# Performance work log

Hardware: AMD Instinct MI355X
Metric: run time of the kernel (lower is better)

Reference implementation:

```python
import jax, jax.numpy as jnp
import numpy as np

B, NOBJ, QD, VD = 128, 36, 2400, 2048
N = B * NOBJ
NEG_SLOPE = 0.2


def _edges():
    # fully connected per image, self-loops included (PyG GATConv adds them)
    base = np.arange(NOBJ)
    src = np.repeat(base, NOBJ)
    dst = np.tile(base, NOBJ)
    off = (np.arange(B) * NOBJ)[:, None]
    return np.stack([(src[None] + off).reshape(-1), (dst[None] + off).reshape(-1)])


def setup_inputs() -> dict:
    key = jax.random.key(0)
    ks = jax.random.split(key, 24)
    p = lambda k, shape, fan: jax.random.normal(k, shape, jnp.float32) * (1.0 / np.sqrt(fan))
    inp = {
        "question_embedding": jax.random.normal(ks[0], (B, QD), jnp.float32),
        "object_features": jax.random.normal(ks[1], (N, VD), jnp.float32),
        "edge_index": jnp.asarray(_edges(), jnp.int32),
        "Wq": p(ks[2], (QD, 2048), QD), "bq": jnp.zeros((2048,), jnp.float32),
        "Wv": p(ks[3], (VD, 2048), VD), "bv": jnp.zeros((2048,), jnp.float32),
        "W1": p(ks[4], (2048, 4 * 256), 2048), "a1s": p(ks[5], (4, 256), 256),
        "a1d": p(ks[6], (4, 256), 256), "b1": jnp.zeros((1024,), jnp.float32),
        "W2": p(ks[7], (1024, 4 * 256), 1024), "a2s": p(ks[8], (4, 256), 256),
        "a2d": p(ks[9], (4, 256), 256), "b2": jnp.zeros((1024,), jnp.float32),
        "W3": p(ks[10], (1024, 5 * 512), 1024), "a3s": p(ks[11], (5, 512), 512),
        "a3d": p(ks[12], (5, 512), 512), "b3": jnp.zeros((512,), jnp.float32),
        "batch_size": B, "num_obj": NOBJ,
    }
    return inp


def gat_conv(x, edge_index, W, a_src, a_dst, b, heads, ch, concat):
    n = x.shape[0]
    h = (x @ W).reshape(n, heads, ch)                       # [N,H,C]
    src, dst = edge_index[0], edge_index[1]
    al_s = jnp.einsum('nhc,hc->nh', h, a_src)               # [N,H]
    al_d = jnp.einsum('nhc,hc->nh', h, a_dst)
    e = jax.nn.leaky_relu(al_s[src] + al_d[dst], NEG_SLOPE)  # [E,H]
    # segment softmax over edges sharing a destination node
    e_max = jax.ops.segment_max(e, dst, num_segments=n)
    e = jnp.exp(e - e_max[dst])
    denom = jax.ops.segment_sum(e, dst, num_segments=n)
    alpha = e / (denom[dst] + 1e-16)                        # [E,H]
    msg = h[src] * alpha[:, :, None]                        # [E,H,C]
    out = jax.ops.segment_sum(msg, dst, num_segments=n)     # [N,H,C]
    out = out.reshape(n, heads * ch) if concat else out.mean(axis=1)
    return out + b


def reference(question_embedding, object_features, edge_index,
              Wq, bq, Wv, bv,
              W1, a1s, a1d, b1,
              W2, a2s, a2d, b2,
              W3, a3s, a3d, b3,
              batch_size, num_obj):
    # hadamard fusion of question with per-object features
    q = question_embedding @ Wq + bq                        # [B,2048]
    q = jnp.repeat(q, num_obj, axis=0)                      # [N,2048]
    v = object_features @ Wv + bv
    x = q * v
    g1 = jax.nn.relu(gat_conv(x, edge_index, W1, a1s, a1d, b1, 4, 256, True))
    g2 = jax.nn.relu(gat_conv(g1, edge_index, W2, a2s, a2d, b2, 4, 256, True))
    g2 = g2 + g1                                            # residual
    return gat_conv(g2, edge_index, W3, a3s, a3d, b3, 5, 512, False)
```

## Files before the change

kernel.cpp:

```cpp
#include <hip/hip_runtime.h>
#include <hip/hip_bf16.h>

typedef unsigned short u16;
typedef __bf16 bf16x8 __attribute__((ext_vector_type(8)));
typedef float f32x4 __attribute__((ext_vector_type(4)));

#define B_IMG 128
#define NOBJ  36
#define NNODE (B_IMG * NOBJ)

__device__ __forceinline__ float b2f(u16 u) {
    union { unsigned int i; float f; } v; v.i = ((unsigned int)u) << 16; return v.f;
}
__device__ __forceinline__ u16 f2b(float f) {
    union { float f; unsigned int i; } v; v.f = f;
    unsigned int u = v.i;
    return (u16)((u + 0x7fffu + ((u >> 16) & 1u)) >> 16);
}

__global__ __launch_bounds__(256)
void conv_mat(const float* __restrict__ src, u16* __restrict__ dst, int n4) {
    const int i = blockIdx.x * 256 + threadIdx.x;
    if (i >= n4) return;
    const float4 f = ((const float4*)src)[i];
    ushort4 o; o.x = f2b(f.x); o.y = f2b(f.y); o.z = f2b(f.z); o.w = f2b(f.w);
    ((ushort4*)dst)[i] = o;
}

__global__ __launch_bounds__(256)
void transpose_cvt(const float* __restrict__ src, u16* __restrict__ dst, int R, int C) {
    __shared__ u16 tile[32][33];
    const int bx = blockIdx.x * 32, by = blockIdx.y * 32;
    const int tx = threadIdx.x & 31, ty = threadIdx.x >> 5;
    #pragma unroll
    for (int i = ty; i < 32; i += 8)
        tile[i][tx] = f2b(src[(size_t)(by + i) * C + bx + tx]);
    __syncthreads();
    #pragma unroll
    for (int i = ty; i < 32; i += 8) dst[(size_t)(bx + i) * R + by + tx] = tile[tx][i];
}

template<int EPI>
__global__ __launch_bounds__(256)
void gemm_tn(const u16* __restrict__ A, const u16* __restrict__ Bt,
             int M, int N, int K, int kLen,
             float* __restrict__ Cf, u16* __restrict__ Cb,
             const float* __restrict__ bias, const float* __restrict__ qmul)
{
    __shared__ __align__(16) u16 lds[3 * 8192];

    const int t    = threadIdx.x;
    const int lane = t & 63;
    const int wave = t >> 6;
    const int wr = wave >> 1, wc = wave & 1;
    const int quad = lane >> 4, l16 = lane & 15;
    const int rowBase = blockIdx.y * 128;
    const int colBase = blockIdx.x * 128;
    const int k0 = blockIdx.z * kLen;

    const u16* gA0 = A  + (size_t)(rowBase + wave * 32 + (lane >> 2)) * K + k0 + (lane & 3) * 8;
    const u16* gA1 = gA0 + 16 * (size_t)K;
    const u16* gB0 = Bt + (size_t)(colBase + wave * 32 + (lane >> 2)) * K + k0 + (lane & 3) * 8;
    const u16* gB1 = gB0 + 16 * (size_t)K;
    const int sO0 = (wave * 32 +  0) * 32;
    const int sO1 = (wave * 32 + 16) * 32;

    int afr[4], bfr[4];
    #pragma unroll
    for (int r = 0; r < 4; r++) afr[r] = (wr * 64 + r * 16 + l16) * 32 + quad * 8;
    #pragma unroll
    for (int c = 0; c < 4; c++) bfr[c] = 4096 + (wc * 64 + c * 16 + l16) * 32 + quad * 8;

    f32x4 acc[4][4];
    #pragma unroll
    for (int r = 0; r < 4; r++)
        #pragma unroll
        for (int c = 0; c < 4; c++)
            acc[r][c] = (f32x4){0.f, 0.f, 0.f, 0.f};

    auto dma_tile = [&](int it, int st) {
        const int kk = it * 32;
        const int bo = st * 8192;
        __builtin_amdgcn_global_load_lds(
            (const __attribute__((address_space(1))) void*)(gA0 + kk),
            (__attribute__((address_space(3))) void*)&lds[bo + sO0], 16, 0, 0);
        __builtin_amdgcn_global_load_lds(
            (const __attribute__((address_space(1))) void*)(gA1 + kk),
            (__attribute__((address_space(3))) void*)&lds[bo + sO1], 16, 0, 0);
        __builtin_amdgcn_global_load_lds(
            (const __attribute__((address_space(1))) void*)(gB0 + kk),
            (__attribute__((address_space(3))) void*)&lds[bo + 4096 + sO0], 16, 0, 0);
        __builtin_amdgcn_global_load_lds(
            (const __attribute__((address_space(1))) void*)(gB1 + kk),
            (__attribute__((address_space(3))) void*)&lds[bo + 4096 + sO1], 16, 0, 0);
    };

    const int nIter = kLen >> 5;
    dma_tile(0, 0);
    dma_tile(1, 1);

    int cur = 0;
    for (int it = 0; it < nIter; ++it) {
        if (it + 1 < nIter) {
            asm volatile("s_waitcnt vmcnt(4)\n\ts_barrier" ::: "memory");
        } else {
            asm volatile("s_waitcnt vmcnt(0)\n\ts_barrier" ::: "memory");
        }
        if (it + 2 < nIter) {
            const int st2 = (cur + 2 >= 3) ? cur - 1 : cur + 2;
            dma_tile(it + 2, st2);
        }
        const int bo = cur * 8192;
        bf16x8 avf[4], bvf[4];
        #pragma unroll
        for (int r = 0; r < 4; r++) avf[r] = *(const bf16x8*)&lds[afr[r] + bo];
        #pragma unroll
        for (int c = 0; c < 4; c++) bvf[c] = *(const bf16x8*)&lds[bfr[c] + bo];
        #pragma unroll
        for (int r = 0; r < 4; r++)
            #pragma unroll
            for (int c = 0; c < 4; c++)
                acc[r][c] = __builtin_amdgcn_mfma_f32_16x16x32_bf16(avf[r], bvf[c], acc[r][c], 0, 0, 0);
        cur = (cur + 1 == 3) ? 0 : cur + 1;
    }

    #pragma unroll
    for (int r = 0; r < 4; r++) {
        const int mBase = rowBase + wr * 64 + r * 16 + quad * 4;
        #pragma unroll
        for (int c = 0; c < 4; c++) {
            const int n = colBase + wc * 64 + c * 16 + l16;
            #pragma unroll
            for (int e = 0; e < 4; e++) {
                const int m = mBase + e;
                float v = acc[r][c][e];
                if (EPI == 1) {
                    Cf[((size_t)blockIdx.z * M + m) * N + n] = v;
                } else if (EPI == 2) {
                    v += bias[n];
                    v *= qmul[(size_t)(m / NOBJ) * N + n];
                    Cb[(size_t)m * N + n] = f2b(v);
                } else {
                    Cb[(size_t)m * N + n] = f2b(v);
                }
            }
        }
    }
}

__global__ __launch_bounds__(256)
void qcombine(const float* __restrict__ p, const float* __restrict__ bias,
              float* __restrict__ q, int MN, int S)
{
    const int i = blockIdx.x * 256 + threadIdx.x;
    float s = 0.f;
    for (int z = 0; z < S; z++) s += p[(size_t)z * MN + i];
    q[i] = s + bias[i & 2047];
}

template<int H, int C>
__global__ __launch_bounds__(H * 64)
void al_kernel(const u16* __restrict__ h, const float* __restrict__ a_s,
               const float* __restrict__ a_d, float* __restrict__ als, float* __restrict__ ald)
{
    const int n = blockIdx.x;
    const int wv = threadIdx.x >> 6, lane = threadIdx.x & 63;
    constexpr int PL = C / 64;
    const u16*   hp  = h   + (size_t)n * (H * C) + wv * C + lane * PL;
    const float* asp = a_s + wv * C + lane * PL;
    const float* adp = a_d + wv * C + lane * PL;
    u16 hb[PL];
    if constexpr (PL == 4) { *(uint2*)hb = *(const uint2*)hp; }
    else                   { *(uint4*)hb = *(const uint4*)hp; }
    float s1 = 0.f, s2 = 0.f;
    #pragma unroll
    for (int i = 0; i < PL; i++) {
        const float hv = b2f(hb[i]);
        s1 += hv * asp[i];
        s2 += hv * adp[i];
    }
    #pragma unroll
    for (int off = 32; off > 0; off >>= 1) {
        s1 += __shfl_down(s1, off);
        s2 += __shfl_down(s2, off);
    }
    if (lane == 0) { als[n * H + wv] = s1; ald[n * H + wv] = s2; }
}

template<int H, int C, int MODE>
__global__ __launch_bounds__(256)
void attn_kernel(const u16* __restrict__ h, const float* __restrict__ a_src,
                 const float* __restrict__ a_dst, const float* __restrict__ bias,
                 const u16* __restrict__ resid, u16* __restrict__ outb)
{
    __shared__ __align__(16) u16 hl[36 * C];
    __shared__ float alpha[36 * 36];
    __shared__ float asl[36], adl[36];
    __shared__ float psum[36][8][2];
    const int b = blockIdx.y, hd = blockIdx.x;
    const int t = threadIdx.x;
    const int nb = b * NOBJ;
    constexpr int CH = C / 8;
    for (int e = t; e < 36 * CH; e += 256) {
        const int row = e / CH, col = (e - row * CH) * 8;
        *(uint4*)&hl[row * C + col] = *(const uint4*)&h[(size_t)(nb + row) * (H * C) + hd * C + col];
    }
    __syncthreads();
    constexpr int SEG = C / 8;
    for (int e = t; e < 36 * 8; e += 256) {
        const int n = e >> 3, sg = e & 7;
        const u16*   hp = &hl[n * C + sg * SEG];
        const float* as = a_src + hd * C + sg * SEG;
        const float* ad = a_dst + hd * C + sg * SEG;
        float s1 = 0.f, s2 = 0.f;
        #pragma unroll 8
        for (int i = 0; i < SEG; i++) {
            const float hv = b2f(hp[i]);
            s1 += hv * as[i]; s2 += hv * ad[i];
        }
        psum[n][sg][0] = s1; psum[n][sg][1] = s2;
    }
    __syncthreads();
    if (t < 36) {
        float s1 = 0.f, s2 = 0.f;
        #pragma unroll
        for (int sg = 0; sg < 8; sg++) { s1 += psum[t][sg][0]; s2 += psum[t][sg][1]; }
        asl[t] = s1; adl[t] = s2;
    }
    __syncthreads();
    if (t < 36) {
        const float ad = adl[t];
        float mx = -1e30f;
        for (int s = 0; s < 36; s++) {
            float v = asl[s] + ad; v = (v > 0.f) ? v : 0.2f * v;
            alpha[t * 36 + s] = v; mx = fmaxf(mx, v);
        }
        float sum = 0.f;
        for (int s = 0; s < 36; s++) { const float ex = expf(alpha[t * 36 + s] - mx); alpha[t * 36 + s] = ex; sum += ex; }
        const float inv = 1.f / (sum + 1e-16f);
        for (int s = 0; s < 36; s++) alpha[t * 36 + s] *= inv;
    }
    __syncthreads();
    constexpr int NC4 = C / 4;
    for (int e = t; e < 36 * NC4; e += 256) {
        const int d = e / NC4, c4 = (e - d * NC4) * 4;
        float a0 = 0, a1 = 0, a2 = 0, a3 = 0;
        for (int s = 0; s < 36; s++) {
            const float al = alpha[d * 36 + s];
            const ushort4 hv = *(const ushort4*)&hl[s * C + c4];
            a0 += al * b2f(hv.x); a1 += al * b2f(hv.y); a2 += al * b2f(hv.z); a3 += al * b2f(hv.w);
        }
        const int n = nb + d;
        const size_t base = (size_t)n * (H * C) + hd * C + c4;
        const int bb = hd * C + c4;
        float v0 = a0 + bias[bb + 0];
        float v1 = a1 + bias[bb + 1];
        float v2 = a2 + bias[bb + 2];
        float v3 = a3 + bias[bb + 3];
        v0 = v0 > 0.f ? v0 : 0.f; v1 = v1 > 0.f ? v1 : 0.f;
        v2 = v2 > 0.f ? v2 : 0.f; v3 = v3 > 0.f ? v3 : 0.f;
        if (MODE == 2) {
            v0 += b2f(resid[base + 0]); v1 += b2f(resid[base + 1]);
            v2 += b2f(resid[base + 2]); v3 += b2f(resid[base + 3]);
        }
        outb[base + 0] = f2b(v0); outb[base + 1] = f2b(v1);
        outb[base + 2] = f2b(v2); outb[base + 3] = f2b(v3);
    }
}

__global__ __launch_bounds__(256)
void attn_mean_kernel(const u16* __restrict__ h, const float* __restrict__ als,
                      const float* __restrict__ ald, const float* __restrict__ b3,
                      float* __restrict__ outp)
{
    __shared__ __align__(16) u16 hl[36 * 256];
    __shared__ float alpha[36 * 36];
    __shared__ float asl[36], adl[36];
    __shared__ float oacc[36 * 256];
    const int b = blockIdx.y, ch = blockIdx.x;
    const int t = threadIdx.x;
    const int nb = b * NOBJ, cbase = ch * 256;
    for (int e = t; e < 36 * 256; e += 256) oacc[e] = 0.f;
    for (int hd = 0; hd < 5; hd++) {
        __syncthreads();
        if (t < 36) { asl[t] = als[(nb + t) * 5 + hd]; adl[t] = ald[(nb + t) * 5 + hd]; }
        for (int e = t; e < 36 * 32; e += 256) {
            const int row = e >> 5, col = (e & 31) * 8;
            *(uint4*)&hl[row * 256 + col] = *(const uint4*)&h[(size_t)(nb + row) * 2560 + hd * 512 + cbase + col];
        }
        __syncthreads();
        if (t < 36) {
            const float ad = adl[t];
            float mx = -1e30f;
            for (int s = 0; s < 36; s++) {
                float v = asl[s] + ad; v = (v > 0.f) ? v : 0.2f * v;
                alpha[t * 36 + s] = v; mx = fmaxf(mx, v);
            }
            float sum = 0.f;
            for (int s = 0; s < 36; s++) { const float ex = expf(alpha[t * 36 + s] - mx); alpha[t * 36 + s] = ex; sum += ex; }
            const float inv = 1.f / (sum + 1e-16f);
            for (int s = 0; s < 36; s++) alpha[t * 36 + s] *= inv;
        }
        __syncthreads();
        for (int e = t; e < 36 * 64; e += 256) {
            const int d = e >> 6, c4 = (e & 63) * 4;
            float a0 = 0, a1 = 0, a2 = 0, a3 = 0;
            for (int s = 0; s < 36; s++) {
                const float al = alpha[d * 36 + s];
                const ushort4 hv = *(const ushort4*)&hl[s * 256 + c4];
                a0 += al * b2f(hv.x); a1 += al * b2f(hv.y); a2 += al * b2f(hv.z); a3 += al * b2f(hv.w);
            }
            oacc[d * 256 + c4 + 0] += a0; oacc[d * 256 + c4 + 1] += a1;
            oacc[d * 256 + c4 + 2] += a2; oacc[d * 256 + c4 + 3] += a3;
        }
    }
    __syncthreads();
    for (int e = t; e < 36 * 64; e += 256) {
        const int d = e >> 6, c4 = (e & 63) * 4;
        #pragma unroll
        for (int j = 0; j < 4; j++)
            outp[(size_t)(nb + d) * 512 + cbase + c4 + j] =
                oacc[d * 256 + c4 + j] * 0.2f + b3[cbase + c4 + j];
    }
}

extern "C" void kernel_launch(void* const* d_in, const int* in_sizes, int n_in,
                              void* d_out, int out_size, void* d_ws, size_t ws_size,
                              hipStream_t stream)
{
    const float* qe  = (const float*)d_in[0];
    const float* of  = (const float*)d_in[1];
    const float* Wq  = (const float*)d_in[3];
    const float* bq  = (const float*)d_in[4];
    const float* Wv  = (const float*)d_in[5];
    const float* bv  = (const float*)d_in[6];
    const float* W1  = (const float*)d_in[7];
    const float* a1s = (const float*)d_in[8];
    const float* a1d = (const float*)d_in[9];
    const float* b1  = (const float*)d_in[10];
    const float* W2  = (const float*)d_in[11];
    const float* a2s = (const float*)d_in[12];
    const float* a2d = (const float*)d_in[13];
    const float* b2  = (const float*)d_in[14];
    const float* W3  = (const float*)d_in[15];
    const float* a3s = (const float*)d_in[16];
    const float* a3d = (const float*)d_in[17];
    const float* b3  = (const float*)d_in[18];
    float* out = (float*)d_out;
    (void)ws_size; (void)in_sizes; (void)n_in; (void)out_size;

    char* W0 = (char*)d_ws;
    size_t off = 0;
    auto alloc = [&](size_t bytes) -> char* {
        char* p = W0 + off; off += (bytes + 255) & ~(size_t)255; return p;
    };
    u16* qe_c = (u16*)alloc(128ull * 2400 * 2);
    u16* of_c = (u16*)alloc(4608ull * 2048 * 2);
    const size_t szA = 4608ull * 2560 * 2;
    const size_t szB = 4608ull * 1024 * 2;
    const size_t szC = 4608ull * 1024 * 2;
    char* Abase = alloc(szA);
    char* Bbase = alloc(szB);
    char* Cbase = alloc(szC);
    char* Dbase = alloc((size_t)NNODE * 5 * 4 * 2);

    u16*   WqT   = (u16*)Abase;
    float* qpart = (float*)(Abase + 2048ull * 2400 * 2);
    u16*   x     = (u16*)Abase;
    u16*   g1    = (u16*)Abase;
    u16*   h3    = (u16*)Abase;
    u16*   WvT   = (u16*)Bbase;
    float* q     = (float*)(Bbase + 2048ull * 2048 * 2);
    u16*   W1T   = (u16*)Bbase;
    u16*   W2T   = (u16*)Bbase;
    u16*   g2    = (u16*)Bbase;
    u16*   h1    = (u16*)Cbase;
    u16*   h2    = (u16*)Cbase;
    u16*   W3T   = (u16*)Cbase;
    float* als   = (float*)Dbase;
    float* ald   = (float*)(Dbase + (size_t)NNODE * 5 * 4);

    conv_mat<<<(128 * 2400 / 4 + 255) / 256, 256, 0, stream>>>(qe, qe_c, 128 * 2400 / 4);
    conv_mat<<<(4608 * 2048 / 4 + 255) / 256, 256, 0, stream>>>(of, of_c, 4608 * 2048 / 4);

    transpose_cvt<<<dim3(64, 75), 256, 0, stream>>>(Wq, WqT, 2400, 2048);
    gemm_tn<1><<<dim3(16, 1, 5), 256, 0, stream>>>(qe_c, WqT, 128, 2048, 2400, 480,
                                                   qpart, nullptr, nullptr, nullptr);
    qcombine<<<dim3(128 * 2048 / 256), 256, 0, stream>>>(qpart, bq, q, 128 * 2048, 5);

    transpose_cvt<<<dim3(64, 64), 256, 0, stream>>>(Wv, WvT, 2048, 2048);
    gemm_tn<2><<<dim3(16, 36, 1), 256, 0, stream>>>(of_c, WvT, 4608, 2048, 2048, 2048,
                                                    nullptr, x, bv, q);

    transpose_cvt<<<dim3(32, 64), 256, 0, stream>>>(W1, W1T, 2048, 1024);
    gemm_tn<0><<<dim3(8, 36, 1), 256, 0, stream>>>(x, W1T, 4608, 1024, 2048, 2048,
                                                   nullptr, h1, nullptr, nullptr);
    attn_kernel<4, 256, 1><<<dim3(4, B_IMG), 256, 0, stream>>>(h1, a1s, a1d, b1, nullptr, g1);

    transpose_cvt<<<dim3(32, 32), 256, 0, stream>>>(W2, W2T, 1024, 1024);
    gemm_tn<0><<<dim3(8, 36, 1), 256, 0, stream>>>(g1, W2T, 4608, 1024, 1024, 1024,
                                                   nullptr, h2, nullptr, nullptr);
    attn_kernel<4, 256, 2><<<dim3(4, B_IMG), 256, 0, stream>>>(h2, a2s, a2d, b2, g1, g2);

    transpose_cvt<<<dim3(80, 32), 256, 0, stream>>>(W3, W3T, 1024, 2560);
    gemm_tn<0><<<dim3(20, 36, 1), 256, 0, stream>>>(g2, W3T, 4608, 2560, 1024, 1024,
                                                    nullptr, h3, nullptr, nullptr);
    al_kernel<5, 512><<<dim3(NNODE), 320, 0, stream>>>(h3, a3s, a3d, als, ald);
    attn_mean_kernel<<<dim3(2, B_IMG), 256, 0, stream>>>(h3, als, ald, b3, out);
}
```

Measured before the change: 474.9 us.

## Switch GEMM to double-buffered 64-wide K stages and zero-pad question K

Result: faster. 453.7 us (-4.5%).

```diff
diff --git a/kernel.cpp b/kernel.cpp
--- a/kernel.cpp
+++ b/kernel.cpp
@@ -28,6 +28,14 @@
 }
 
 __global__ __launch_bounds__(256)
+void conv_pad_qe(const float* __restrict__ src, u16* __restrict__ dst) {
+    const int i = blockIdx.x * 256 + threadIdx.x;
+    if (i >= 128 * 2560) return;
+    const int r = i / 2560, c = i - r * 2560;
+    dst[i] = (c < 2400) ? f2b(src[r * 2400 + c]) : (u16)0;
+}
+
+__global__ __launch_bounds__(256)
 void transpose_cvt(const float* __restrict__ src, u16* __restrict__ dst, int R, int C) {
     __shared__ u16 tile[32][33];
     const int bx = blockIdx.x * 32, by = blockIdx.y * 32;
@@ -40,6 +48,21 @@
     for (int i = ty; i < 32; i += 8) dst[(size_t)(bx + i) * R + by + tx] = tile[tx][i];
 }
 
+__global__ __launch_bounds__(256)
+void transpose_cvt_padK(const float* __restrict__ src, u16* __restrict__ dst) {
+    __shared__ u16 tile[32][33];
+    const int bx = blockIdx.x * 32, by = blockIdx.y * 32;
+    const int tx = threadIdx.x & 31, ty = threadIdx.x >> 5;
+    #pragma unroll
+    for (int i = ty; i < 32; i += 8) {
+        const int k = by + i;
+        tile[i][tx] = (k < 2400) ? f2b(src[(size_t)k * 2048 + bx + tx]) : (u16)0;
+    }
+    __syncthreads();
+    #pragma unroll
+    for (int i = ty; i < 32; i += 8) dst[(size_t)(bx + i) * 2560 + by + tx] = tile[tx][i];
+}
+
 template<int EPI>
 __global__ __launch_bounds__(256)
 void gemm_tn(const u16* __restrict__ A, const u16* __restrict__ Bt,
@@ -47,7 +70,7 @@
              float* __restrict__ Cf, u16* __restrict__ Cb,
              const float* __restrict__ bias, const float* __restrict__ qmul)
 {
-    __shared__ __align__(16) u16 lds[3 * 8192];
+    __shared__ __align__(16) u16 lds[2 * 16384];
 
     const int t    = threadIdx.x;
     const int lane = t & 63;
@@ -62,14 +85,13 @@
     const u16* gA1 = gA0 + 16 * (size_t)K;
     const u16* gB0 = Bt + (size_t)(colBase + wave * 32 + (lane >> 2)) * K + k0 + (lane & 3) * 8;
     const u16* gB1 = gB0 + 16 * (size_t)K;
-    const int sO0 = (wave * 32 +  0) * 32;
-    const int sO1 = (wave * 32 + 16) * 32;
+    const int ro = wave * 1024;
 
     int afr[4], bfr[4];
     #pragma unroll
     for (int r = 0; r < 4; r++) afr[r] = (wr * 64 + r * 16 + l16) * 32 + quad * 8;
     #pragma unroll
-    for (int c = 0; c < 4; c++) bfr[c] = 4096 + (wc * 64 + c * 16 + l16) * 32 + quad * 8;
+    for (int c = 0; c < 4; c++) bfr[c] = 8192 + (wc * 64 + c * 16 + l16) * 32 + quad * 8;
 
     f32x4 acc[4][4];
     #pragma unroll
@@ -78,50 +100,45 @@
         for (int c = 0; c < 4; c++)
             acc[r][c] = (f32x4){0.f, 0.f, 0.f, 0.f};
 
-    auto dma_tile = [&](int it, int st) {
-        const int kk = it * 32;
-        const int bo = st * 8192;
+    auto gld = [](const u16* g, u16* s) {
         __builtin_amdgcn_global_load_lds(
-            (const __attribute__((address_space(1))) void*)(gA0 + kk),
-            (__attribute__((address_space(3))) void*)&lds[bo + sO0], 16, 0, 0);
-        __builtin_amdgcn_global_load_lds(
-            (const __attribute__((address_space(1))) void*)(gA1 + kk),
-            (__attribute__((address_space(3))) void*)&lds[bo + sO1], 16, 0, 0);
-        __builtin_amdgcn_global_load_lds(
-            (const __attribute__((address_space(1))) void*)(gB0 + kk),
-            (__attribute__((address_space(3))) void*)&lds[bo + 4096 + sO0], 16, 0, 0);
-        __builtin_amdgcn_global_load_lds(
-            (const __attribute__((address_space(1))) void*)(gB1 + kk),
-            (__attribute__((address_space(3))) void*)&lds[bo + 4096 + sO1], 16, 0, 0);
+            (const __attribute__((address_space(1))) void*)g,
+            (__attribute__((address_space(3))) void*)s, 16, 0, 0);
     };
-
-    const int nIter = kLen >> 5;
-    dma_tile(0, 0);
-    dma_tile(1, 1);
-
-    int cur = 0;
+    auto dma_stage = [&](int it, int st) {
+        const int kk = it * 64;
+        const int bo = st * 16384;
+        gld(gA0 + kk,      &lds[bo + ro]);
+        gld(gA1 + kk,      &lds[bo + ro + 512]);
+        gld(gA0 + kk + 32, &lds[bo + 4096 + ro]);
+        gld(gA1 + kk + 32, &lds[bo + 4096 + ro + 512]);
+        gld(gB0 + kk,      &lds[bo + 8192 + ro]);
+        gld(gB1 + kk,      &lds[bo + 8192 + ro + 512]);
+        gld(gB0 + kk + 32, &lds[bo + 12288 + ro]);
+        gld(gB1 + kk + 32, &lds[bo + 12288 + ro + 512]);
+    };
+
+    const int nIter = kLen >> 6;
+    dma_stage(0, 0);
+
     for (int it = 0; it < nIter; ++it) {
-        if (it + 1 < nIter) {
-            asm volatile("s_waitcnt vmcnt(4)\n\ts_barrier" ::: "memory");
-        } else {
-            asm volatile("s_waitcnt vmcnt(0)\n\ts_barrier" ::: "memory");
-        }
-        if (it + 2 < nIter) {
-            const int st2 = (cur + 2 >= 3) ? cur - 1 : cur + 2;
-            dma_tile(it + 2, st2);
-        }
-        const int bo = cur * 8192;
-        bf16x8 avf[4], bvf[4];
+        asm volatile("s_waitcnt vmcnt(0)\n\ts_barrier" ::: "memory");
+        if (it + 1 < nIter) dma_stage(it + 1, (it + 1) & 1);
+        const int bo = (it & 1) * 16384;
         #pragma unroll
-        for (int r = 0; r < 4; r++) avf[r] = *(const bf16x8*)&lds[afr[r] + bo];
-        #pragma unroll
-        for (int c = 0; c < 4; c++) bvf[c] = *(const bf16x8*)&lds[bfr[c] + bo];
-        #pragma unroll
-        for (int r = 0; r < 4; r++)
+        for (int j = 0; j < 2; j++) {
+            const int so = bo + j * 4096;
+            bf16x8 avf[4], bvf[4];
             #pragma unroll
-            for (int c = 0; c < 4; c++)
-                acc[r][c] = __builtin_amdgcn_mfma_f32_16x16x32_bf16(avf[r], bvf[c], acc[r][c], 0, 0, 0);
-        cur = (cur + 1 == 3) ? 0 : cur + 1;
+            for (int r = 0; r < 4; r++) avf[r] = *(const bf16x8*)&lds[so + afr[r]];
+            #pragma unroll
+            for (int c = 0; c < 4; c++) bvf[c] = *(const bf16x8*)&lds[so + bfr[c]];
+            #pragma unroll
+            for (int r = 0; r < 4; r++)
+                #pragma unroll
+                for (int c = 0; c < 4; c++)
+                    acc[r][c] = __builtin_amdgcn_mfma_f32_16x16x32_bf16(avf[r], bvf[c], acc[r][c], 0, 0, 0);
+        }
     }
 
     #pragma unroll
@@ -354,7 +371,7 @@
     auto alloc = [&](size_t bytes) -> char* {
         char* p = W0 + off; off += (bytes + 255) & ~(size_t)255; return p;
     };
-    u16* qe_c = (u16*)alloc(128ull * 2400 * 2);
+    u16* qe_c = (u16*)alloc(128ull * 2560 * 2);
     u16* of_c = (u16*)alloc(4608ull * 2048 * 2);
     const size_t szA = 4608ull * 2560 * 2;
     const size_t szB = 4608ull * 1024 * 2;
@@ -365,7 +382,7 @@
     char* Dbase = alloc((size_t)NNODE * 5 * 4 * 2);
 
     u16*   WqT   = (u16*)Abase;
-    float* qpart = (float*)(Abase + 2048ull * 2400 * 2);
+    float* qpart = (float*)(Abase + 2048ull * 2560 * 2);
     u16*   x     = (u16*)Abase;
     u16*   g1    = (u16*)Abase;
     u16*   h3    = (u16*)Abase;
@@ -380,11 +397,11 @@
     float* als   = (float*)Dbase;
     float* ald   = (float*)(Dbase + (size_t)NNODE * 5 * 4);
 
-    conv_mat<<<(128 * 2400 / 4 + 255) / 256, 256, 0, stream>>>(qe, qe_c, 128 * 2400 / 4);
+    conv_pad_qe<<<(128 * 2560 + 255) / 256, 256, 0, stream>>>(qe, qe_c);
     conv_mat<<<(4608 * 2048 / 4 + 255) / 256, 256, 0, stream>>>(of, of_c, 4608 * 2048 / 4);
 
-    transpose_cvt<<<dim3(64, 75), 256, 0, stream>>>(Wq, WqT, 2400, 2048);
-    gemm_tn<1><<<dim3(16, 1, 5), 256, 0, stream>>>(qe_c, WqT, 128, 2048, 2400, 480,
+    transpose_cvt_padK<<<dim3(64, 80), 256, 0, stream>>>(Wq, WqT);
+    gemm_tn<1><<<dim3(16, 1, 5), 256, 0, stream>>>(qe_c, WqT, 128, 2048, 2560, 512,
                                                    qpart, nullptr, nullptr, nullptr);
     qcombine<<<dim3(128 * 2048 / 256), 256, 0, stream>>>(qpart, bq, q, 128 * 2048, 5);
 
```
